# Kernel optimization log

Hardware: AMD Instinct MI355X
Metric: run time of the kernel (lower is better)

## Reference

```python
import jax, jax.numpy as jnp
import numpy as np
from jax import lax

D_MODEL = 512
EXPAND = 2
INNER = D_MODEL * EXPAND
K = 4
B, T = 8, 2048
LN_EPS = 1e-5


def setup_inputs() -> dict:
    key = jax.random.key(0)
    ks = jax.random.split(key, 12)
    s_in = 1.0 / np.sqrt(D_MODEL)
    s_out = 1.0 / np.sqrt(INNER)
    return {
        "x": jax.random.normal(ks[0], (B, T, D_MODEL), dtype=jnp.float32),
        "ln_w": jnp.ones((D_MODEL,), jnp.float32),
        "ln_b": jnp.zeros((D_MODEL,), jnp.float32),
        "in_proj_w": jax.random.uniform(ks[1], (3 * INNER, D_MODEL), jnp.float32, -s_in, s_in),
        "in_proj_b": jax.random.uniform(ks[2], (3 * INNER,), jnp.float32, -s_in, s_in),
        "conv_w": jax.random.uniform(ks[3], (INNER, 1, K), jnp.float32, -0.5, 0.5),
        "conv_b": jax.random.uniform(ks[4], (INNER,), jnp.float32, -0.5, 0.5),
        "delta_w": jax.random.uniform(ks[5], (INNER, D_MODEL), jnp.float32, -s_in, s_in),
        "delta_b": jax.random.uniform(ks[6], (INNER,), jnp.float32, -s_in, s_in),
        "state_mix": jnp.zeros((INNER,), jnp.float32),
        "skip_scale": jnp.ones((INNER,), jnp.float32),
        "out_proj_w": jax.random.uniform(ks[7], (D_MODEL, INNER), jnp.float32, -s_out, s_out),
        "out_proj_b": jax.random.uniform(ks[8], (D_MODEL,), jnp.float32, -s_out, s_out),
    }


def _layernorm(x, w, b):
    mu = jnp.mean(x, axis=-1, keepdims=True)
    var = jnp.mean(jnp.square(x - mu), axis=-1, keepdims=True)
    return (x - mu) * lax.rsqrt(var + LN_EPS) * w + b


def _causal_dw_conv(x_bct, w, b):
    # x: [B, C, T], w: [C, 1, K] depthwise, left pad K-1 (causal)
    y = lax.conv_general_dilated(
        x_bct, w, window_strides=(1,), padding=[(K - 1, 0)],
        dimension_numbers=("NCH", "OIH", "NCH"), feature_group_count=INNER)
    return y + b[None, :, None]


def reference(x, ln_w, ln_b, in_proj_w, in_proj_b, conv_w, conv_b,
              delta_w, delta_b, state_mix, skip_scale, out_proj_w, out_proj_b):
    residual = x
    xn = _layernorm(x, ln_w, ln_b)                      # [B,T,D]
    h = xn @ in_proj_w.T + in_proj_b                     # [B,T,3*INNER]
    proj, gate, drive = jnp.split(h, 3, axis=-1)
    proj = jax.nn.silu(proj)
    gate = jax.nn.sigmoid(gate)
    conv_out = _causal_dw_conv(jnp.swapaxes(proj, 1, 2), conv_w, conv_b)
    conv_out = jnp.swapaxes(conv_out, 1, 2)              # [B,T,INNER]
    delta = jnp.maximum(jax.nn.sigmoid(xn @ delta_w.T + delta_b), 1e-4)
    drive = jnp.tanh(drive)
    a = jax.nn.sigmoid(state_mix)                        # [INNER]
    d = delta * drive                                    # [B,T,INNER]

    def step(state, d_t):
        state = a * state + d_t
        return state, state

    _, states = lax.scan(step, jnp.zeros((x.shape[0], INNER), x.dtype),
                         jnp.swapaxes(d, 0, 1))          # [T,B,INNER]
    states = jnp.swapaxes(states, 0, 1)                  # [B,T,INNER]
    y = (states + skip_scale * conv_out) * gate
    y = y @ out_proj_w.T + out_proj_b
    return residual + y
```

## Files before the change

### kernel.cpp

```cpp
#include <hip/hip_runtime.h>
#include <stdint.h>

#define D_MODEL 512
#define INNER   1024
#define NCAT    4096
#define BATCH   8
#define SEQ     2048
#define ROWS    (BATCH*SEQ)
#define LN_EPS  1e-5f
#define CHUNK   64
#define NCHUNK  (SEQ/CHUNK)

typedef unsigned short u16;
typedef unsigned int   u32;
typedef __attribute__((ext_vector_type(8))) short bf16x8;
typedef __attribute__((ext_vector_type(4))) float f32x4;

__device__ __forceinline__ u16 f2bf(float f) {
  u32 u = __builtin_bit_cast(u32, f);
  return (u16)((u + 0x7FFFu + ((u >> 16) & 1u)) >> 16);
}
__device__ __forceinline__ float bf2f(u32 lo) {
  return __builtin_bit_cast(float, lo << 16);
}
__device__ __forceinline__ float sigf(float x){ return 1.f/(1.f+__expf(-x)); }

__device__ __forceinline__ void glds16(const void* g, void* l) {
  __builtin_amdgcn_global_load_lds((const __attribute__((address_space(1))) void*)g,
                                   (__attribute__((address_space(3))) void*)l, 16, 0, 0);
}

__global__ __launch_bounds__(256) void ln_kernel(const float* __restrict__ x,
    const float* __restrict__ lw, const float* __restrict__ lb,
    u16* __restrict__ xn) {
  const int row  = blockIdx.x * 4 + (threadIdx.x >> 6);
  const int lane = threadIdx.x & 63;
  const float4* xr = (const float4*)(x + (size_t)row * D_MODEL);
  float4 v0 = xr[lane*2], v1 = xr[lane*2+1];
  float s  = v0.x+v0.y+v0.z+v0.w + v1.x+v1.y+v1.z+v1.w;
  float s2 = v0.x*v0.x+v0.y*v0.y+v0.z*v0.z+v0.w*v0.w
           + v1.x*v1.x+v1.y*v1.y+v1.z*v1.z+v1.w*v1.w;
  #pragma unroll
  for (int o=32;o;o>>=1){ s += __shfl_xor(s,o); s2 += __shfl_xor(s2,o); }
  const float mu = s * (1.f/D_MODEL);
  const float rs = rsqrtf(s2*(1.f/D_MODEL) - mu*mu + LN_EPS);
  const float4* wv = (const float4*)lw; const float4* bv = (const float4*)lb;
  float4 w0 = wv[lane*2], w1 = wv[lane*2+1];
  float4 b0 = bv[lane*2], b1 = bv[lane*2+1];
  u32 p0 = (u32)f2bf((v0.x-mu)*rs*w0.x+b0.x) | ((u32)f2bf((v0.y-mu)*rs*w0.y+b0.y)<<16);
  u32 p1 = (u32)f2bf((v0.z-mu)*rs*w0.z+b0.z) | ((u32)f2bf((v0.w-mu)*rs*w0.w+b0.w)<<16);
  u32 p2 = (u32)f2bf((v1.x-mu)*rs*w1.x+b1.x) | ((u32)f2bf((v1.y-mu)*rs*w1.y+b1.y)<<16);
  u32 p3 = (u32)f2bf((v1.z-mu)*rs*w1.z+b1.z) | ((u32)f2bf((v1.w-mu)*rs*w1.w+b1.w)<<16);
  ((uint4*)(xn + (size_t)row * D_MODEL))[lane] = make_uint4(p0,p1,p2,p3);
}

__global__ void cvt_kernel(const float* __restrict__ s, u16* __restrict__ d, int n) {
  for (int i = blockIdx.x*blockDim.x+threadIdx.x; i < n; i += gridDim.x*blockDim.x)
    d[i] = f2bf(s[i]);
}

__device__ __forceinline__ void sched_blk(int nbm, int nbn, int GM, int GN,
                                          int& bM, int& bN) {
  const int nwg = nbm * nbn;
  const int bid = blockIdx.x;
  const int cpx = nwg >> 3;
  const int swz = (bid & 7) * cpx + (bid >> 3);
  const int gsz = GM * GN;
  const int g   = swz / gsz, loc = swz - g * gsz;
  const int ngn = nbn / GN;
  const int gm  = g / ngn,  gn  = g - gm * ngn;
  bM = gm * GM + (loc % GM);
  bN = gn * GN + (loc / GM);
}

__device__ __forceinline__ void gemm_main(const u16* __restrict__ A,
    const u16* __restrict__ Bm, int K, int nkt, int bM, int bN,
    u16* lA, u16* lB, f32x4 acc[4][4]) {
  const int tid = threadIdx.x;
  const int l6  = tid >> 2;
  const int sg  = (tid & 3) ^ (l6 & 3);
  const int pB  = (l6 & 15) * 4 + ((l6 >> 4) & 3);
  const u16* gA = A  + (size_t)(bM*128 + l6)*K + sg*8;
  const u16* gB = Bm + (size_t)(bN*128 + pB)*K + sg*8;
  u16* dA = lA + tid*8;
  u16* dB = lB + tid*8;
  const size_t rstep = (size_t)64*K;

#define STAGE_T(koff, bufo) do { \
    const u16* sA = gA + (koff); const u16* sB = gB + (koff); \
    glds16(sA,         dA + (bufo));        glds16(sA + rstep, dA + (bufo) + 2048); \
    glds16(sB,         dB + (bufo));        glds16(sB + rstep, dB + (bufo) + 2048); \
  } while (0)

  STAGE_T(0, 0);
  STAGE_T(32, 4096);
  asm volatile("s_waitcnt vmcnt(4)" ::: "memory");
  __builtin_amdgcn_s_barrier();

  const int lane = tid & 63, wv = tid >> 6;
  const int wm = wv >> 1, wn = wv & 1;
  const int kx = ((lane>>4) ^ (lane&3)) * 8;
  const int aoff = (wm*64 + (lane&15))*32 + kx;
  const int boff = (wn*64 + (lane&15))*32 + kx;

  int cur = 0, stg = 8192;
  for (int kt = 0; kt < nkt; ++kt) {
    bf16x8 af[4], bfr[4];
    #pragma unroll
    for (int m=0;m<4;m++) af[m]  = *(const bf16x8*)&lA[cur + aoff + m*512];
    #pragma unroll
    for (int n=0;n<4;n++) bfr[n] = *(const bf16x8*)&lB[cur + boff + n*512];
    asm volatile("s_waitcnt lgkmcnt(0)" ::: "memory");
    __builtin_amdgcn_sched_barrier(0);
    __builtin_amdgcn_s_barrier();
    if (kt + 2 < nkt) STAGE_T((kt+2)*32, stg);
    #pragma unroll
    for (int m=0;m<4;m++)
      #pragma unroll
      for (int n=0;n<4;n++)
        acc[m][n] = __builtin_amdgcn_mfma_f32_16x16x32_bf16(af[m], bfr[n], acc[m][n], 0,0,0);
    if (kt + 2 < nkt) { asm volatile("s_waitcnt vmcnt(4)" ::: "memory"); }
    else              { asm volatile("s_waitcnt vmcnt(0)" ::: "memory"); }
    __builtin_amdgcn_s_barrier();
    cur += 4096; if (cur == 12288) cur = 0;
    stg += 4096; if (stg == 12288) stg = 0;
  }
#undef STAGE_T
}

__global__ __launch_bounds__(256, 3) void gemm1_kernel(const u16* __restrict__ A,
    const u16* __restrict__ Bm, const float* __restrict__ ipb,
    const float* __restrict__ db, u16* __restrict__ proj, u16* __restrict__ gate,
    u16* __restrict__ drive, u16* __restrict__ delta) {
  __shared__ u16 lA[12288], lB[12288];
  f32x4 acc[4][4];
  #pragma unroll
  for (int m=0;m<4;m++)
    #pragma unroll
    for (int n=0;n<4;n++) acc[m][n] = (f32x4){0.f,0.f,0.f,0.f};
  int bM, bN; sched_blk(ROWS/128, NCAT/128, 16, 8, bM, bN);
  gemm_main(A, Bm, D_MODEL, D_MODEL/32, bM, bN, lA, lB, acc);
  const int lane = threadIdx.x & 63, wv = threadIdx.x >> 6;
  const int wm = wv>>1, wn = wv&1;
  const int g = (bN*128) >> 10;
  u16* outp = (g==0)?proj:(g==1)?gate:(g==2)?drive:delta;
  const int colb = bN*128 + wn*64 + (lane&15)*4;
  const float4 b4 = (colb < 3072) ? *(const float4*)&ipb[colb]
                                  : *(const float4*)&db[colb-3072];
  const float* bp = (const float*)&b4;
  const int lcolb = colb & (INNER-1);
  #pragma unroll
  for (int m=0;m<4;m++) {
    const int row0 = bM*128 + wm*64 + m*16 + ((lane>>4)<<2);
    #pragma unroll
    for (int r=0;r<4;r++) {
      float a[4];
      #pragma unroll
      for (int n=0;n<4;n++) {
        float v = acc[m][n][r] + bp[n];
        if (g==0)      a[n] = v * sigf(v);
        else if (g==1) a[n] = sigf(v);
        else if (g==2) a[n] = 2.f*sigf(2.f*v) - 1.f;
        else           a[n] = fmaxf(sigf(v), 1e-4f);
      }
      u32 lo = (u32)f2bf(a[0]) | ((u32)f2bf(a[1])<<16);
      u32 hi = (u32)f2bf(a[2]) | ((u32)f2bf(a[3])<<16);
      *(uint2*)&outp[(size_t)(row0+r)*INNER + lcolb] = make_uint2(lo, hi);
    }
  }
}

__global__ __launch_bounds__(256, 3) void gemm2_kernel(const u16* __restrict__ A,
    const u16* __restrict__ Bm, const float* __restrict__ ob,
    const float* __restrict__ resid, float* __restrict__ out) {
  __shared__ u16 lA[12288], lB[12288];
  f32x4 acc[4][4];
  #pragma unroll
  for (int m=0;m<4;m++)
    #pragma unroll
    for (int n=0;n<4;n++) acc[m][n] = (f32x4){0.f,0.f,0.f,0.f};
  int bM, bN; sched_blk(ROWS/128, D_MODEL/128, 8, 4, bM, bN);
  gemm_main(A, Bm, INNER, INNER/32, bM, bN, lA, lB, acc);
  const int lane = threadIdx.x & 63, wv = threadIdx.x >> 6;
  const int wm = wv>>1, wn = wv&1;
  const int colb = bN*128 + wn*64 + (lane&15)*4;
  const float4 ob4 = *(const float4*)&ob[colb];
  #pragma unroll
  for (int m=0;m<4;m++) {
    const int row0 = bM*128 + wm*64 + m*16 + ((lane>>4)<<2);
    #pragma unroll
    for (int r=0;r<4;r++) {
      const size_t idx = (size_t)(row0+r)*D_MODEL + colb;
      float4 rs = *(const float4*)&resid[idx];
      float4 o;
      o.x = acc[m][0][r] + ob4.x + rs.x;
      o.y = acc[m][1][r] + ob4.y + rs.y;
      o.z = acc[m][2][r] + ob4.z + rs.z;
      o.w = acc[m][3][r] + ob4.w + rs.w;
      *(float4*)&out[idx] = o;
    }
  }
}

__global__ __launch_bounds__(256) void scan1_kernel(const u16* __restrict__ delta,
    const u16* __restrict__ drive, const float* __restrict__ sm,
    float* __restrict__ cS) {
  const int blk = blockIdx.x;
  const int half = blk & 1, ch = (blk>>1) & (NCHUNK-1), b = blk >> 6;
  const int c0 = half*512 + threadIdx.x*2;
  const float a0 = sigf(sm[c0]), a1 = sigf(sm[c0+1]);
  float s0 = 0.f, s1 = 0.f;
  size_t base = ((size_t)b*SEQ + ch*CHUNK)*INNER + c0;
  for (int t=0;t<CHUNK;t++) {
    u32 dl = *(const u32*)(delta + base);
    u32 dv = *(const u32*)(drive + base);
    s0 = a0*s0 + bf2f(dl & 0xffffu)*bf2f(dv & 0xffffu);
    s1 = a1*s1 + bf2f(dl >> 16)*bf2f(dv >> 16);
    base += INNER;
  }
  const size_t o = ((size_t)b*NCHUNK + ch)*INNER + c0;
  cS[o] = s0; cS[o+1] = s1;
}

__global__ __launch_bounds__(256) void scan2_kernel(const float* __restrict__ sm,
    const float* __restrict__ cS, float* __restrict__ carry) {
  const int idx = blockIdx.x*256 + threadIdx.x;
  const int b = idx >> 9, c0 = (idx & 511)*2;
  const float a0 = sigf(sm[c0]), a1 = sigf(sm[c0+1]);
  float A0 = a0, A1 = a1;
  #pragma unroll
  for (int i=0;i<6;i++){ A0*=A0; A1*=A1; }
  float cr0 = 0.f, cr1 = 0.f;
  for (int ch=0; ch<NCHUNK; ch++) {
    const size_t o = ((size_t)b*NCHUNK + ch)*INNER + c0;
    carry[o] = cr0; carry[o+1] = cr1;
    cr0 = A0*cr0 + cS[o];
    cr1 = A1*cr1 + cS[o+1];
  }
}

__global__ __launch_bounds__(256) void scan3_kernel(const u16* __restrict__ proj,
    const u16* __restrict__ gate, const u16* __restrict__ delta,
    const u16* __restrict__ drive, const float* __restrict__ carry,
    const float* __restrict__ sm, const float* __restrict__ cw,
    const float* __restrict__ cb, const float* __restrict__ sk,
    u16* __restrict__ z) {
  const int blk = blockIdx.x;
  const int half = blk & 1, ch = (blk>>1) & (NCHUNK-1), b = blk >> 6;
  const int c0 = half*512 + threadIdx.x*2;
  const float a0 = sigf(sm[c0]), a1 = sigf(sm[c0+1]);
  const float cb0 = cb[c0], cb1 = cb[c0+1];
  const float sk0 = sk[c0], sk1 = sk[c0+1];
  const float w00=cw[c0*4+0], w01=cw[c0*4+1], w02=cw[c0*4+2], w03=cw[c0*4+3];
  const float w10=cw[c0*4+4], w11=cw[c0*4+5], w12=cw[c0*4+6], w13=cw[c0*4+7];
  const size_t o = ((size_t)b*NCHUNK + ch)*INNER + c0;
  float s0 = carry[o], s1 = carry[o+1];
  const int t0 = ch*CHUNK;
  const size_t rowb = (size_t)b*SEQ*INNER + c0;
  float pa0=0,pb0=0,pc0=0, pa1=0,pb1=0,pc1=0;
  if (ch > 0) {
    u32 u3 = *(const u32*)(proj + rowb + (size_t)(t0-3)*INNER);
    u32 u2 = *(const u32*)(proj + rowb + (size_t)(t0-2)*INNER);
    u32 u1 = *(const u32*)(proj + rowb + (size_t)(t0-1)*INNER);
    pa0 = bf2f(u3&0xffffu); pa1 = bf2f(u3>>16);
    pb0 = bf2f(u2&0xffffu); pb1 = bf2f(u2>>16);
    pc0 = bf2f(u1&0xffffu); pc1 = bf2f(u1>>16);
  }
  size_t base = rowb + (size_t)t0*INNER;
  for (int t=0;t<CHUNK;t++) {
    u32 pu = *(const u32*)(proj + base);
    const float pd0 = bf2f(pu&0xffffu), pd1 = bf2f(pu>>16);
    const float co0 = w00*pa0 + w01*pb0 + w02*pc0 + w03*pd0 + cb0;
    const float co1 = w10*pa1 + w11*pb1 + w12*pc1 + w13*pd1 + cb1;
    pa0=pb0; pb0=pc0; pc0=pd0;  pa1=pb1; pb1=pc1; pc1=pd1;
    u32 dl = *(const u32*)(delta + base);
    u32 dv = *(const u32*)(drive + base);
    s0 = a0*s0 + bf2f(dl&0xffffu)*bf2f(dv&0xffffu);
    s1 = a1*s1 + bf2f(dl>>16)*bf2f(dv>>16);
    u32 gu = *(const u32*)(gate + base);
    const float z0 = (s0 + sk0*co0)*bf2f(gu&0xffffu);
    const float z1 = (s1 + sk1*co1)*bf2f(gu>>16);
    *(u32*)(z + base) = (u32)f2bf(z0) | ((u32)f2bf(z1)<<16);
    base += INNER;
  }
}

extern "C" void kernel_launch(void* const* d_in, const int* in_sizes, int n_in,
                              void* d_out, int out_size, void* d_ws, size_t ws_size,
                              hipStream_t stream) {
  const float* x    = (const float*)d_in[0];
  const float* ln_w = (const float*)d_in[1];
  const float* ln_b = (const float*)d_in[2];
  const float* ipw  = (const float*)d_in[3];
  const float* ipb  = (const float*)d_in[4];
  const float* cw   = (const float*)d_in[5];
  const float* cb   = (const float*)d_in[6];
  const float* dw   = (const float*)d_in[7];
  const float* db   = (const float*)d_in[8];
  const float* sm   = (const float*)d_in[9];
  const float* sk   = (const float*)d_in[10];
  const float* opw  = (const float*)d_in[11];
  const float* opb  = (const float*)d_in[12];
  float* out = (float*)d_out;

  uint8_t* w = (uint8_t*)d_ws;
  u16* xn    = (u16*)w;  w += (size_t)ROWS*D_MODEL*2;
  u16* wcat  = (u16*)w;  w += (size_t)NCAT*D_MODEL*2;
  u16* wout  = (u16*)w;  w += (size_t)D_MODEL*INNER*2;
  u16* proj  = (u16*)w;  w += (size_t)ROWS*INNER*2;
  u16* gate  = (u16*)w;  w += (size_t)ROWS*INNER*2;
  u16* drv   = (u16*)w;  w += (size_t)ROWS*INNER*2;
  u16* dlt   = (u16*)w;  w += (size_t)ROWS*INNER*2;
  u16* z     = (u16*)w;  w += (size_t)ROWS*INNER*2;
  float* cS    = (float*)w; w += (size_t)BATCH*NCHUNK*INNER*4;
  float* carry = (float*)w; w += (size_t)BATCH*NCHUNK*INNER*4;

  ln_kernel<<<ROWS/4, 256, 0, stream>>>(x, ln_w, ln_b, xn);
  cvt_kernel<<<2048, 256, 0, stream>>>(ipw, wcat, 3072*512);
  cvt_kernel<<<1024, 256, 0, stream>>>(dw, wcat + (size_t)3072*512, 1024*512);
  cvt_kernel<<<1024, 256, 0, stream>>>(opw, wout, 512*1024);
  gemm1_kernel<<<(ROWS/128)*(NCAT/128), 256, 0, stream>>>(xn, wcat, ipb, db, proj, gate, drv, dlt);
  scan1_kernel<<<BATCH*NCHUNK*2, 256, 0, stream>>>(dlt, drv, sm, cS);
  scan2_kernel<<<16, 256, 0, stream>>>(sm, cS, carry);
  scan3_kernel<<<BATCH*NCHUNK*2, 256, 0, stream>>>(proj, gate, dlt, drv, carry, sm, cw, cb, sk, z);
  gemm2_kernel<<<(ROWS/128)*(D_MODEL/128), 256, 0, stream>>>(z, wout, opb, x, out);
}
```

Measured before the change: 195.6 us.

## Rewrite gemm1 with 256x256 tiles, 8 waves and phased ping-pong LDS schedule

```diff
diff --git a/kernel.cpp b/kernel.cpp
--- a/kernel.cpp
+++ b/kernel.cpp
@@ -29,6 +29,8 @@
   __builtin_amdgcn_global_load_lds((const __attribute__((address_space(1))) void*)g,
                                    (__attribute__((address_space(3))) void*)l, 16, 0, 0);
 }
+
+#define MFMA16(a,b,c) __builtin_amdgcn_mfma_f32_16x16x32_bf16((a),(b),(c),0,0,0)
 
 __global__ __launch_bounds__(256) void ln_kernel(const float* __restrict__ x,
     const float* __restrict__ lw, const float* __restrict__ lb,
@@ -73,6 +75,152 @@
   bN = gn * GN + (loc / GM);
 }
 
+__global__ __launch_bounds__(512, 2) void gemm1_kernel(const u16* __restrict__ A,
+    const u16* __restrict__ Bm, const float* __restrict__ ipb,
+    const float* __restrict__ db, u16* __restrict__ proj, u16* __restrict__ gate,
+    u16* __restrict__ drive, u16* __restrict__ delta) {
+  extern __shared__ u16 lds[];
+  const int tid = threadIdx.x;
+  int bM, bN; sched_blk(ROWS/256, NCAT/256, 8, 4, bM, bN);
+
+  const int rS = tid >> 3;
+  const int cS = (tid & 7) ^ (rS & 7);
+  const int pB = (rS & 15) * 4 + (rS >> 4);
+  const u16* gA = A  + (size_t)(bM*256 + rS)*D_MODEL + cS*8;
+  const u16* gB = Bm + (size_t)(bN*256 + pB)*D_MODEL + cS*8;
+  u16* dA = lds + tid*8;
+  u16* dB = lds + 16384 + tid*8;
+
+#define STAGE_A(SLOT, KT) do { const u16* s_ = gA + (KT)*64; u16* d_ = dA + (SLOT); \
+    glds16(s_, d_); glds16(s_+64*D_MODEL, d_+4096); \
+    glds16(s_+128*D_MODEL, d_+8192); glds16(s_+192*D_MODEL, d_+12288); } while(0)
+#define STAGE_B(SLOT, KT) do { const u16* s_ = gB + (KT)*64; u16* d_ = dB + (SLOT); \
+    glds16(s_, d_); glds16(s_+64*D_MODEL, d_+4096); \
+    glds16(s_+128*D_MODEL, d_+8192); glds16(s_+192*D_MODEL, d_+12288); } while(0)
+
+  const int lane = tid & 63, wid = tid >> 6;
+  const int wm = wid >> 2, wn = wid & 3;
+  const int kx0 = ((lane>>4) ^ (lane&7)) * 8;
+  const int kx1 = kx0 ^ 32;
+  const int aW0 = wm*8192 + (lane&15)*64 + kx0;
+  const int aW1 = wm*8192 + (lane&15)*64 + kx1;
+  const int bWc = 16384 + (wn>>1)*8192 + (wn&1)*4096 + (lane&15)*64;
+  const int bW0 = bWc + kx0, bW1 = bWc + kx1;
+
+  f32x4 acc[8][4];
+  #pragma unroll
+  for (int m=0;m<8;m++)
+    #pragma unroll
+    for (int n=0;n<4;n++) acc[m][n] = (f32x4){0.f,0.f,0.f,0.f};
+  bf16x8 af[4][2], bf[4][2];
+
+  STAGE_A(0, 0); STAGE_B(0, 0);
+  asm volatile("s_waitcnt vmcnt(0)" ::: "memory");
+  __builtin_amdgcn_s_barrier();
+
+#define WAIT_PHASE do { \
+    asm volatile("s_waitcnt lgkmcnt(0)" ::: "memory"); \
+    __builtin_amdgcn_sched_barrier(0); \
+    __builtin_amdgcn_s_barrier(); \
+    __builtin_amdgcn_s_setprio(1); } while(0)
+#define END_PHASE do { \
+    __builtin_amdgcn_s_setprio(0); \
+    __builtin_amdgcn_s_barrier(); } while(0)
+
+  #pragma unroll 2
+  for (int kt = 0; kt < 8; ++kt) {
+    const int sb = (kt & 1) << 15;
+    const int nb = sb ^ 32768;
+    #pragma unroll
+    for (int mm=0; mm<4; ++mm) {
+      af[mm][0] = *(const bf16x8*)&lds[sb + aW0 + mm*1024];
+      af[mm][1] = *(const bf16x8*)&lds[sb + aW1 + mm*1024];
+    }
+    bf[0][0] = *(const bf16x8*)&lds[sb + bW0];
+    bf[0][1] = *(const bf16x8*)&lds[sb + bW1];
+    bf[1][0] = *(const bf16x8*)&lds[sb + bW0 + 1024];
+    bf[1][1] = *(const bf16x8*)&lds[sb + bW1 + 1024];
+    if (kt < 7) STAGE_A(nb, kt+1);
+    WAIT_PHASE;
+    #pragma unroll
+    for (int mm=0;mm<4;++mm) {
+      acc[mm][0] = MFMA16(af[mm][0], bf[0][0], acc[mm][0]);
+      acc[mm][0] = MFMA16(af[mm][1], bf[0][1], acc[mm][0]);
+      acc[mm][1] = MFMA16(af[mm][0], bf[1][0], acc[mm][1]);
+      acc[mm][1] = MFMA16(af[mm][1], bf[1][1], acc[mm][1]);
+    }
+    END_PHASE;
+    bf[2][0] = *(const bf16x8*)&lds[sb + bW0 + 2048];
+    bf[2][1] = *(const bf16x8*)&lds[sb + bW1 + 2048];
+    bf[3][0] = *(const bf16x8*)&lds[sb + bW0 + 3072];
+    bf[3][1] = *(const bf16x8*)&lds[sb + bW1 + 3072];
+    if (kt < 7) STAGE_B(nb, kt+1);
+    WAIT_PHASE;
+    #pragma unroll
+    for (int mm=0;mm<4;++mm) {
+      acc[mm][2] = MFMA16(af[mm][0], bf[2][0], acc[mm][2]);
+      acc[mm][2] = MFMA16(af[mm][1], bf[2][1], acc[mm][2]);
+      acc[mm][3] = MFMA16(af[mm][0], bf[3][0], acc[mm][3]);
+      acc[mm][3] = MFMA16(af[mm][1], bf[3][1], acc[mm][3]);
+    }
+    END_PHASE;
+    #pragma unroll
+    for (int mm=0; mm<4; ++mm) {
+      af[mm][0] = *(const bf16x8*)&lds[sb + aW0 + 4096 + mm*1024];
+      af[mm][1] = *(const bf16x8*)&lds[sb + aW1 + 4096 + mm*1024];
+    }
+    WAIT_PHASE;
+    #pragma unroll
+    for (int mm=0;mm<4;++mm) {
+      acc[4+mm][2] = MFMA16(af[mm][0], bf[2][0], acc[4+mm][2]);
+      acc[4+mm][2] = MFMA16(af[mm][1], bf[2][1], acc[4+mm][2]);
+      acc[4+mm][3] = MFMA16(af[mm][0], bf[3][0], acc[4+mm][3]);
+      acc[4+mm][3] = MFMA16(af[mm][1], bf[3][1], acc[4+mm][3]);
+    }
+    END_PHASE;
+    __builtin_amdgcn_s_setprio(1);
+    #pragma unroll
+    for (int mm=0;mm<4;++mm) {
+      acc[4+mm][0] = MFMA16(af[mm][0], bf[0][0], acc[4+mm][0]);
+      acc[4+mm][0] = MFMA16(af[mm][1], bf[0][1], acc[4+mm][0]);
+      acc[4+mm][1] = MFMA16(af[mm][0], bf[1][0], acc[4+mm][1]);
+      acc[4+mm][1] = MFMA16(af[mm][1], bf[1][1], acc[4+mm][1]);
+    }
+    __builtin_amdgcn_s_setprio(0);
+    asm volatile("s_waitcnt vmcnt(0)" ::: "memory");
+    __builtin_amdgcn_s_barrier();
+  }
+#undef STAGE_A
+#undef STAGE_B
+
+  const int g = bN >> 2;
+  u16* outp = (g==0)?proj:(g==1)?gate:(g==2)?drive:delta;
+  const int colb = bN*256 + wn*64 + (lane&15)*4;
+  const float4 b4 = (colb < 3072) ? *(const float4*)&ipb[colb]
+                                  : *(const float4*)&db[colb-3072];
+  const float* bp = (const float*)&b4;
+  const int lcolb = colb & (INNER-1);
+  #pragma unroll
+  for (int m=0;m<8;m++) {
+    const int row0 = bM*256 + wm*128 + m*16 + ((lane>>4)<<2);
+    #pragma unroll
+    for (int r=0;r<4;r++) {
+      float a4[4];
+      #pragma unroll
+      for (int n=0;n<4;n++) {
+        float v = acc[m][n][r] + bp[n];
+        if (g==0)      a4[n] = v * sigf(v);
+        else if (g==1) a4[n] = sigf(v);
+        else if (g==2) a4[n] = 2.f*sigf(2.f*v) - 1.f;
+        else           a4[n] = fmaxf(sigf(v), 1e-4f);
+      }
+      u32 lo = (u32)f2bf(a4[0]) | ((u32)f2bf(a4[1])<<16);
+      u32 hi = (u32)f2bf(a4[2]) | ((u32)f2bf(a4[3])<<16);
+      *(uint2*)&outp[(size_t)(row0+r)*INNER + lcolb] = make_uint2(lo, hi);
+    }
+  }
+}
+
 __device__ __forceinline__ void gemm_main(const u16* __restrict__ A,
     const u16* __restrict__ Bm, int K, int nkt, int bM, int bN,
     u16* lA, u16* lB, f32x4 acc[4][4]) {
@@ -118,7 +266,7 @@
     for (int m=0;m<4;m++)
       #pragma unroll
       for (int n=0;n<4;n++)
-        acc[m][n] = __builtin_amdgcn_mfma_f32_16x16x32_bf16(af[m], bfr[n], acc[m][n], 0,0,0);
+        acc[m][n] = MFMA16(af[m], bfr[n], acc[m][n]);
     if (kt + 2 < nkt) { asm volatile("s_waitcnt vmcnt(4)" ::: "memory"); }
     else              { asm volatile("s_waitcnt vmcnt(0)" ::: "memory"); }
     __builtin_amdgcn_s_barrier();
@@ -126,48 +274,6 @@
     stg += 4096; if (stg == 12288) stg = 0;
   }
 #undef STAGE_T
-}
-
-__global__ __launch_bounds__(256, 3) void gemm1_kernel(const u16* __restrict__ A,
-    const u16* __restrict__ Bm, const float* __restrict__ ipb,
-    const float* __restrict__ db, u16* __restrict__ proj, u16* __restrict__ gate,
-    u16* __restrict__ drive, u16* __restrict__ delta) {
-  __shared__ u16 lA[12288], lB[12288];
-  f32x4 acc[4][4];
-  #pragma unroll
-  for (int m=0;m<4;m++)
-    #pragma unroll
-    for (int n=0;n<4;n++) acc[m][n] = (f32x4){0.f,0.f,0.f,0.f};
-  int bM, bN; sched_blk(ROWS/128, NCAT/128, 16, 8, bM, bN);
-  gemm_main(A, Bm, D_MODEL, D_MODEL/32, bM, bN, lA, lB, acc);
-  const int lane = threadIdx.x & 63, wv = threadIdx.x >> 6;
-  const int wm = wv>>1, wn = wv&1;
-  const int g = (bN*128) >> 10;
-  u16* outp = (g==0)?proj:(g==1)?gate:(g==2)?drive:delta;
-  const int colb = bN*128 + wn*64 + (lane&15)*4;
-  const float4 b4 = (colb < 3072) ? *(const float4*)&ipb[colb]
-                                  : *(const float4*)&db[colb-3072];
-  const float* bp = (const float*)&b4;
-  const int lcolb = colb & (INNER-1);
-  #pragma unroll
-  for (int m=0;m<4;m++) {
-    const int row0 = bM*128 + wm*64 + m*16 + ((lane>>4)<<2);
-    #pragma unroll
-    for (int r=0;r<4;r++) {
-      float a[4];
-      #pragma unroll
-      for (int n=0;n<4;n++) {
-        float v = acc[m][n][r] + bp[n];
-        if (g==0)      a[n] = v * sigf(v);
-        else if (g==1) a[n] = sigf(v);
-        else if (g==2) a[n] = 2.f*sigf(2.f*v) - 1.f;
-        else           a[n] = fmaxf(sigf(v), 1e-4f);
-      }
-      u32 lo = (u32)f2bf(a[0]) | ((u32)f2bf(a[1])<<16);
-      u32 hi = (u32)f2bf(a[2]) | ((u32)f2bf(a[3])<<16);
-      *(uint2*)&outp[(size_t)(row0+r)*INNER + lcolb] = make_uint2(lo, hi);
-    }
-  }
 }
 
 __global__ __launch_bounds__(256, 3) void gemm2_kernel(const u16* __restrict__ A,
@@ -319,7 +425,7 @@
   cvt_kernel<<<2048, 256, 0, stream>>>(ipw, wcat, 3072*512);
   cvt_kernel<<<1024, 256, 0, stream>>>(dw, wcat + (size_t)3072*512, 1024*512);
   cvt_kernel<<<1024, 256, 0, stream>>>(opw, wout, 512*1024);
-  gemm1_kernel<<<(ROWS/128)*(NCAT/128), 256, 0, stream>>>(xn, wcat, ipb, db, proj, gate, drv, dlt);
+  gemm1_kernel<<<(ROWS/256)*(NCAT/256), 512, 131072, stream>>>(xn, wcat, ipb, db, proj, gate, drv, dlt);
   scan1_kernel<<<BATCH*NCHUNK*2, 256, 0, stream>>>(dlt, drv, sm, cS);
   scan2_kernel<<<16, 256, 0, stream>>>(sm, cS, carry);
   scan3_kernel<<<BATCH*NCHUNK*2, 256, 0, stream>>>(proj, gate, dlt, drv, carry, sm, cw, cb, sk, z);
```

After: 228.0 us. +16.6%, slower.

## Fuse delta*drive into GEMM1 epilogue via interleaved weights; merge weight conversions

Applied to the files above, without the earlier changes.

```diff
diff --git a/kernel.cpp b/kernel.cpp
--- a/kernel.cpp
+++ b/kernel.cpp
@@ -29,6 +29,8 @@
   __builtin_amdgcn_global_load_lds((const __attribute__((address_space(1))) void*)g,
                                    (__attribute__((address_space(3))) void*)l, 16, 0, 0);
 }
+
+#define MFMA16(a,b,c) __builtin_amdgcn_mfma_f32_16x16x32_bf16((a),(b),(c),0,0,0)
 
 __global__ __launch_bounds__(256) void ln_kernel(const float* __restrict__ x,
     const float* __restrict__ lw, const float* __restrict__ lb,
@@ -54,9 +56,30 @@
   ((uint4*)(xn + (size_t)row * D_MODEL))[lane] = make_uint4(p0,p1,p2,p3);
 }
 
-__global__ void cvt_kernel(const float* __restrict__ s, u16* __restrict__ d, int n) {
-  for (int i = blockIdx.x*blockDim.x+threadIdx.x; i < n; i += gridDim.x*blockDim.x)
-    d[i] = f2bf(s[i]);
+__global__ __launch_bounds__(256) void cvt_all_kernel(const float* __restrict__ ipw,
+    const float* __restrict__ dw, const float* __restrict__ opw,
+    const float* __restrict__ ipb, const float* __restrict__ db,
+    u16* __restrict__ wcat, u16* __restrict__ wout, float* __restrict__ bcat) {
+  const int i = blockIdx.x*256 + threadIdx.x;
+  const int NW1 = NCAT*D_MODEL, NW2 = D_MODEL*INNER, STR = gridDim.x*256;
+  for (int idx = i; idx < NW1; idx += STR) {
+    const int r = idx >> 9, c = idx & 511;
+    float v;
+    if (r < 2048) v = ipw[idx];
+    else {
+      const int rr = r - 2048;
+      v = (rr & 1) ? dw[(size_t)(rr>>1)*D_MODEL + c]
+                   : ipw[(size_t)(2048 + (rr>>1))*D_MODEL + c];
+    }
+    wcat[idx] = f2bf(v);
+  }
+  for (int idx = i; idx < NW2; idx += STR) wout[idx] = f2bf(opw[idx]);
+  if (i < NCAT) {
+    float b;
+    if (i < 2048) b = ipb[i];
+    else { const int rr = i - 2048; b = (rr & 1) ? db[rr>>1] : ipb[2048 + (rr>>1)]; }
+    bcat[i] = b;
+  }
 }
 
 __device__ __forceinline__ void sched_blk(int nbm, int nbn, int GM, int GN,
@@ -96,6 +119,7 @@
   STAGE_T(32, 4096);
   asm volatile("s_waitcnt vmcnt(4)" ::: "memory");
   __builtin_amdgcn_s_barrier();
+  __builtin_amdgcn_sched_barrier(0);
 
   const int lane = tid & 63, wv = tid >> 6;
   const int wm = wv >> 1, wn = wv & 1;
@@ -110,18 +134,16 @@
     for (int m=0;m<4;m++) af[m]  = *(const bf16x8*)&lA[cur + aoff + m*512];
     #pragma unroll
     for (int n=0;n<4;n++) bfr[n] = *(const bf16x8*)&lB[cur + boff + n*512];
-    asm volatile("s_waitcnt lgkmcnt(0)" ::: "memory");
-    __builtin_amdgcn_sched_barrier(0);
-    __builtin_amdgcn_s_barrier();
     if (kt + 2 < nkt) STAGE_T((kt+2)*32, stg);
     #pragma unroll
     for (int m=0;m<4;m++)
       #pragma unroll
       for (int n=0;n<4;n++)
-        acc[m][n] = __builtin_amdgcn_mfma_f32_16x16x32_bf16(af[m], bfr[n], acc[m][n], 0,0,0);
+        acc[m][n] = MFMA16(af[m], bfr[n], acc[m][n]);
     if (kt + 2 < nkt) { asm volatile("s_waitcnt vmcnt(4)" ::: "memory"); }
     else              { asm volatile("s_waitcnt vmcnt(0)" ::: "memory"); }
     __builtin_amdgcn_s_barrier();
+    __builtin_amdgcn_sched_barrier(0);
     cur += 4096; if (cur == 12288) cur = 0;
     stg += 4096; if (stg == 12288) stg = 0;
   }
@@ -129,9 +151,8 @@
 }
 
 __global__ __launch_bounds__(256, 3) void gemm1_kernel(const u16* __restrict__ A,
-    const u16* __restrict__ Bm, const float* __restrict__ ipb,
-    const float* __restrict__ db, u16* __restrict__ proj, u16* __restrict__ gate,
-    u16* __restrict__ drive, u16* __restrict__ delta) {
+    const u16* __restrict__ Bm, const float* __restrict__ bcat,
+    u16* __restrict__ proj, u16* __restrict__ gate, u16* __restrict__ dbuf) {
   __shared__ u16 lA[12288], lB[12288];
   f32x4 acc[4][4];
   #pragma unroll
@@ -142,30 +163,43 @@
   gemm_main(A, Bm, D_MODEL, D_MODEL/32, bM, bN, lA, lB, acc);
   const int lane = threadIdx.x & 63, wv = threadIdx.x >> 6;
   const int wm = wv>>1, wn = wv&1;
-  const int g = (bN*128) >> 10;
-  u16* outp = (g==0)?proj:(g==1)?gate:(g==2)?drive:delta;
   const int colb = bN*128 + wn*64 + (lane&15)*4;
-  const float4 b4 = (colb < 3072) ? *(const float4*)&ipb[colb]
-                                  : *(const float4*)&db[colb-3072];
+  const float4 b4 = *(const float4*)&bcat[colb];
   const float* bp = (const float*)&b4;
-  const int lcolb = colb & (INNER-1);
-  #pragma unroll
-  for (int m=0;m<4;m++) {
-    const int row0 = bM*128 + wm*64 + m*16 + ((lane>>4)<<2);
-    #pragma unroll
-    for (int r=0;r<4;r++) {
-      float a[4];
+  if (colb < 2048) {
+    u16* outp = (colb < 1024) ? proj : gate;
+    const int lcolb = colb & (INNER-1);
+    #pragma unroll
+    for (int m=0;m<4;m++) {
+      const int row0 = bM*128 + wm*64 + m*16 + ((lane>>4)<<2);
       #pragma unroll
-      for (int n=0;n<4;n++) {
-        float v = acc[m][n][r] + bp[n];
-        if (g==0)      a[n] = v * sigf(v);
-        else if (g==1) a[n] = sigf(v);
-        else if (g==2) a[n] = 2.f*sigf(2.f*v) - 1.f;
-        else           a[n] = fmaxf(sigf(v), 1e-4f);
+      for (int r=0;r<4;r++) {
+        float a4[4];
+        #pragma unroll
+        for (int n=0;n<4;n++) {
+          float v = acc[m][n][r] + bp[n];
+          a4[n] = (colb < 1024) ? v * sigf(v) : sigf(v);
+        }
+        u32 lo = (u32)f2bf(a4[0]) | ((u32)f2bf(a4[1])<<16);
+        u32 hi = (u32)f2bf(a4[2]) | ((u32)f2bf(a4[3])<<16);
+        *(uint2*)&outp[(size_t)(row0+r)*INNER + lcolb] = make_uint2(lo, hi);
       }
-      u32 lo = (u32)f2bf(a[0]) | ((u32)f2bf(a[1])<<16);
-      u32 hi = (u32)f2bf(a[2]) | ((u32)f2bf(a[3])<<16);
-      *(uint2*)&outp[(size_t)(row0+r)*INNER + lcolb] = make_uint2(lo, hi);
+    }
+  } else {
+    const int ch0 = (colb - 2048) >> 1;
+    #pragma unroll
+    for (int m=0;m<4;m++) {
+      const int row0 = bM*128 + wm*64 + m*16 + ((lane>>4)<<2);
+      #pragma unroll
+      for (int r=0;r<4;r++) {
+        const float v0 = acc[m][0][r] + bp[0];
+        const float v1 = acc[m][1][r] + bp[1];
+        const float v2 = acc[m][2][r] + bp[2];
+        const float v3 = acc[m][3][r] + bp[3];
+        const float d0 = (2.f*sigf(2.f*v0) - 1.f) * fmaxf(sigf(v1), 1e-4f);
+        const float d1 = (2.f*sigf(2.f*v2) - 1.f) * fmaxf(sigf(v3), 1e-4f);
+        *(u32*)&dbuf[(size_t)(row0+r)*INNER + ch0] = (u32)f2bf(d0) | ((u32)f2bf(d1)<<16);
+      }
     }
   }
 }
@@ -202,9 +236,8 @@
   }
 }
 
-__global__ __launch_bounds__(256) void scan1_kernel(const u16* __restrict__ delta,
-    const u16* __restrict__ drive, const float* __restrict__ sm,
-    float* __restrict__ cS) {
+__global__ __launch_bounds__(256) void scan1_kernel(const u16* __restrict__ d,
+    const float* __restrict__ sm, float* __restrict__ cS) {
   const int blk = blockIdx.x;
   const int half = blk & 1, ch = (blk>>1) & (NCHUNK-1), b = blk >> 6;
   const int c0 = half*512 + threadIdx.x*2;
@@ -212,10 +245,9 @@
   float s0 = 0.f, s1 = 0.f;
   size_t base = ((size_t)b*SEQ + ch*CHUNK)*INNER + c0;
   for (int t=0;t<CHUNK;t++) {
-    u32 dl = *(const u32*)(delta + base);
-    u32 dv = *(const u32*)(drive + base);
-    s0 = a0*s0 + bf2f(dl & 0xffffu)*bf2f(dv & 0xffffu);
-    s1 = a1*s1 + bf2f(dl >> 16)*bf2f(dv >> 16);
+    u32 du = *(const u32*)(d + base);
+    s0 = a0*s0 + bf2f(du & 0xffffu);
+    s1 = a1*s1 + bf2f(du >> 16);
     base += INNER;
   }
   const size_t o = ((size_t)b*NCHUNK + ch)*INNER + c0;
@@ -240,11 +272,10 @@
 }
 
 __global__ __launch_bounds__(256) void scan3_kernel(const u16* __restrict__ proj,
-    const u16* __restrict__ gate, const u16* __restrict__ delta,
-    const u16* __restrict__ drive, const float* __restrict__ carry,
-    const float* __restrict__ sm, const float* __restrict__ cw,
-    const float* __restrict__ cb, const float* __restrict__ sk,
-    u16* __restrict__ z) {
+    const u16* __restrict__ gate, const u16* __restrict__ d,
+    const float* __restrict__ carry, const float* __restrict__ sm,
+    const float* __restrict__ cw, const float* __restrict__ cb,
+    const float* __restrict__ sk, u16* __restrict__ z) {
   const int blk = blockIdx.x;
   const int half = blk & 1, ch = (blk>>1) & (NCHUNK-1), b = blk >> 6;
   const int c0 = half*512 + threadIdx.x*2;
@@ -273,10 +304,9 @@
     const float co0 = w00*pa0 + w01*pb0 + w02*pc0 + w03*pd0 + cb0;
     const float co1 = w10*pa1 + w11*pb1 + w12*pc1 + w13*pd1 + cb1;
     pa0=pb0; pb0=pc0; pc0=pd0;  pa1=pb1; pb1=pc1; pc1=pd1;
-    u32 dl = *(const u32*)(delta + base);
-    u32 dv = *(const u32*)(drive + base);
-    s0 = a0*s0 + bf2f(dl&0xffffu)*bf2f(dv&0xffffu);
-    s1 = a1*s1 + bf2f(dl>>16)*bf2f(dv>>16);
+    u32 du = *(const u32*)(d + base);
+    s0 = a0*s0 + bf2f(du&0xffffu);
+    s1 = a1*s1 + bf2f(du>>16);
     u32 gu = *(const u32*)(gate + base);
     const float z0 = (s0 + sk0*co0)*bf2f(gu&0xffffu);
     const float z1 = (s1 + sk1*co1)*bf2f(gu>>16);
@@ -309,19 +339,17 @@
   u16* wout  = (u16*)w;  w += (size_t)D_MODEL*INNER*2;
   u16* proj  = (u16*)w;  w += (size_t)ROWS*INNER*2;
   u16* gate  = (u16*)w;  w += (size_t)ROWS*INNER*2;
-  u16* drv   = (u16*)w;  w += (size_t)ROWS*INNER*2;
-  u16* dlt   = (u16*)w;  w += (size_t)ROWS*INNER*2;
+  u16* dbuf  = (u16*)w;  w += (size_t)ROWS*INNER*2;
   u16* z     = (u16*)w;  w += (size_t)ROWS*INNER*2;
   float* cS    = (float*)w; w += (size_t)BATCH*NCHUNK*INNER*4;
   float* carry = (float*)w; w += (size_t)BATCH*NCHUNK*INNER*4;
+  float* bcat  = (float*)w; w += (size_t)NCAT*4;
 
   ln_kernel<<<ROWS/4, 256, 0, stream>>>(x, ln_w, ln_b, xn);
-  cvt_kernel<<<2048, 256, 0, stream>>>(ipw, wcat, 3072*512);
-  cvt_kernel<<<1024, 256, 0, stream>>>(dw, wcat + (size_t)3072*512, 1024*512);
-  cvt_kernel<<<1024, 256, 0, stream>>>(opw, wout, 512*1024);
-  gemm1_kernel<<<(ROWS/128)*(NCAT/128), 256, 0, stream>>>(xn, wcat, ipb, db, proj, gate, drv, dlt);
-  scan1_kernel<<<BATCH*NCHUNK*2, 256, 0, stream>>>(dlt, drv, sm, cS);
+  cvt_all_kernel<<<1024, 256, 0, stream>>>(ipw, dw, opw, ipb, db, wcat, wout, bcat);
+  gemm1_kernel<<<(ROWS/128)*(NCAT/128), 256, 0, stream>>>(xn, wcat, bcat, proj, gate, dbuf);
+  scan1_kernel<<<BATCH*NCHUNK*2, 256, 0, stream>>>(dbuf, sm, cS);
   scan2_kernel<<<16, 256, 0, stream>>>(sm, cS, carry);
-  scan3_kernel<<<BATCH*NCHUNK*2, 256, 0, stream>>>(proj, gate, dlt, drv, carry, sm, cw, cb, sk, z);
+  scan3_kernel<<<BATCH*NCHUNK*2, 256, 0, stream>>>(proj, gate, dbuf, carry, sm, cw, cb, sk, z);
   gemm2_kernel<<<(ROWS/128)*(D_MODEL/128), 256, 0, stream>>>(z, wout, opb, x, out);
 }
```

Result: faster. 168.1 us (-14.1%).
